# Kernel tuning notes

Measured on AMD Instinct MI355X. Metric: run time of the kernel, lower is better.

Reference implementation:

```python
import jax, jax.numpy as jnp
import numpy as np

D_MODEL = 512
H = 8
D_FF = 2048
EPS = 1e-6
NEG_INF = -1.0e9


def setup_inputs() -> dict:
    key = jax.random.key(0)
    ks = jax.random.split(key, 12)
    B, S, D, F = 8, 2048, D_MODEL, D_FF
    s = 0.02
    inp = {
        "x": jax.random.normal(ks[0], (B, S, D), jnp.float32),
        "src_mask": jnp.ones((B, 1, 1, S), jnp.int32),
        "w_q": jax.random.normal(ks[1], (D, D), jnp.float32) * s,
        "b_q": jnp.zeros((D,), jnp.float32),
        "w_k": jax.random.normal(ks[2], (D, D), jnp.float32) * s,
        "b_k": jnp.zeros((D,), jnp.float32),
        "w_v": jax.random.normal(ks[3], (D, D), jnp.float32) * s,
        "b_v": jnp.zeros((D,), jnp.float32),
        "w_o": jax.random.normal(ks[4], (D, D), jnp.float32) * s,
        "b_o": jnp.zeros((D,), jnp.float32),
        "w_1": jax.random.normal(ks[5], (F, D), jnp.float32) * s,
        "b_1": jnp.zeros((F,), jnp.float32),
        "w_2": jax.random.normal(ks[6], (D, F), jnp.float32) * s,
        "b_2": jnp.zeros((D,), jnp.float32),
    }
    return inp


def _layer_norm(x):
    # Matches torch: (x - mu) / sqrt(std**2 + eps), std is UNBIASED (ddof=1);
    # alpha/bias params exist in the module but are never applied in forward.
    mu = jnp.mean(x, axis=-1, keepdims=True)
    var = jnp.var(x, axis=-1, keepdims=True, ddof=1)
    return (x - mu) / jnp.sqrt(var + EPS)


def _mha(x, src_mask, w_q, b_q, w_k, b_k, w_v, b_v, w_o, b_o):
    B, S, D = x.shape
    d_k = D // H
    q = x @ w_q.T + b_q
    k = x @ w_k.T + b_k
    v = x @ w_v.T + b_v
    # (B, S, H, d_k) -> (B, H, S, d_k)
    q = q.reshape(B, S, H, d_k).transpose(0, 2, 1, 3)
    k = k.reshape(B, S, H, d_k).transpose(0, 2, 1, 3)
    v = v.reshape(B, S, H, d_k).transpose(0, 2, 1, 3)
    scores = jnp.einsum("bhqd,bhkd->bhqk", q, k) / jnp.sqrt(jnp.float32(d_k))
    scores = jnp.where(src_mask == 0, NEG_INF, scores)
    attn = jax.nn.softmax(scores, axis=-1)  # (B, H, S, S) materialized, as in source
    out = jnp.einsum("bhqk,bhkd->bhqd", attn, v)
    out = out.transpose(0, 2, 1, 3).reshape(B, S, D)
    return out @ w_o.T + b_o


def _ffn(x, w_1, b_1, w_2, b_2):
    return jax.nn.relu(x @ w_1.T + b_1) @ w_2.T + b_2


def reference(x, src_mask, w_q, b_q, w_k, b_k, w_v, b_v, w_o, b_o, w_1, b_1, w_2, b_2):
    # dropout prob = 0.0 -> identity (eval-equivalent)
    x1 = x + _mha(_layer_norm(x), src_mask, w_q, b_q, w_k, b_k, w_v, b_v, w_o, b_o)
    return x1 + _ffn(_layer_norm(x1), w_1, b_1, w_2, b_2)
```

## Files before the change

### kernel.cpp

```cpp
#include <hip/hip_runtime.h>
#include <hip/hip_bf16.h>

typedef unsigned short u16;
typedef __bf16 bf16x8 __attribute__((ext_vector_type(8)));
typedef __bf16 bf16x4 __attribute__((ext_vector_type(4)));
typedef unsigned int u32x4 __attribute__((ext_vector_type(4)));
typedef float f32x4 __attribute__((ext_vector_type(4)));

#define SEQ 2048
#define DMODEL 512
#define NHEAD 8
#define DFF 2048
#define NBATCH 8
#define MROWS (NBATCH * SEQ)

#define C1_FOLD 0.18033688f

__device__ __forceinline__ u16 f2b(float f) {
    __hip_bfloat16 h = __float2bfloat16(f);
    u16 u;
    __builtin_memcpy(&u, &h, 2);
    return u;
}

__device__ __forceinline__ unsigned int pack2(float a, float b) {
    float2 f{a, b};
    __hip_bfloat162 h = __float22bfloat162_rn(f);
    unsigned int u;
    __builtin_memcpy(&u, &h, 4);
    return u;
}

__device__ __forceinline__ float ex2(float x) {
#if __has_builtin(__builtin_amdgcn_exp2f)
    return __builtin_amdgcn_exp2f(x);
#else
    return exp2f(x);
#endif
}

__device__ __forceinline__ void gload_lds16(const void* g, void* lds) {
    auto* gp = reinterpret_cast<const __attribute__((address_space(1))) unsigned int*>(
        reinterpret_cast<uintptr_t>(g));
    auto* lp = reinterpret_cast<__attribute__((address_space(3))) unsigned int*>(
        reinterpret_cast<uintptr_t>(lds));
    __builtin_amdgcn_global_load_lds(gp, lp, 16, 0, 0);
}

__global__ __launch_bounds__(256) void cast_weights(
    const float* __restrict__ w0, const float* __restrict__ w1,
    const float* __restrict__ w2, const float* __restrict__ w3,
    const float* __restrict__ w4, const float* __restrict__ w5,
    u16* __restrict__ d0, u16* __restrict__ d1, u16* __restrict__ d2,
    u16* __restrict__ d3, u16* __restrict__ d4, u16* __restrict__ d5) {
    int blk = blockIdx.x;
    const float* s;
    u16* d;
    int base;
    float sc = 1.0f;
    if (blk < 512) {
        int seg = blk >> 7, lb = blk & 127;
        s = seg == 0 ? w0 : seg == 1 ? w1 : seg == 2 ? w2 : w3;
        d = seg == 0 ? d0 : seg == 1 ? d1 : seg == 2 ? d2 : d3;
        base = lb * 2048;
        if (seg == 0) sc = C1_FOLD;
    } else if (blk < 1024) {
        s = w4; d = d4; base = (blk - 512) * 2048;
    } else {
        s = w5; d = d5; base = (blk - 1024) * 2048;
    }
    int i = base + threadIdx.x * 8;
    float4 a = *reinterpret_cast<const float4*>(s + i);
    float4 b = *reinterpret_cast<const float4*>(s + i + 4);
    ushort4 oa, ob;
    oa.x = f2b(a.x * sc); oa.y = f2b(a.y * sc);
    oa.z = f2b(a.z * sc); oa.w = f2b(a.w * sc);
    ob.x = f2b(b.x * sc); ob.y = f2b(b.y * sc);
    ob.z = f2b(b.z * sc); ob.w = f2b(b.w * sc);
    *reinterpret_cast<ushort4*>(d + i) = oa;
    *reinterpret_cast<ushort4*>(d + i + 4) = ob;
}

__global__ __launch_bounds__(256) void concat_bias(const float* __restrict__ bq,
                                                   const float* __restrict__ bk,
                                                   const float* __restrict__ bv,
                                                   float* __restrict__ dst) {
    int i = blockIdx.x * 256 + threadIdx.x;
    float v = i < 512 ? bq[i] * C1_FOLD : (i < 1024 ? bk[i - 512] : bv[i - 1024]);
    dst[i] = v;
}

__global__ __launch_bounds__(256) void ln_rows(const float* __restrict__ x,
                                               u16* __restrict__ out) {
    int row = blockIdx.x * 4 + (threadIdx.x >> 6);
    int l = threadIdx.x & 63;
    const float* xr = x + (size_t)row * DMODEL + l * 8;
    float4 a = *reinterpret_cast<const float4*>(xr);
    float4 b = *reinterpret_cast<const float4*>(xr + 4);
    float s = a.x + a.y + a.z + a.w + b.x + b.y + b.z + b.w;
    float q = a.x * a.x + a.y * a.y + a.z * a.z + a.w * a.w +
              b.x * b.x + b.y * b.y + b.z * b.z + b.w * b.w;
#pragma unroll
    for (int d = 32; d >= 1; d >>= 1) {
        s += __shfl_xor(s, d, 64);
        q += __shfl_xor(q, d, 64);
    }
    float mean = s * (1.f / 512.f);
    float var = (q - 512.f * mean * mean) * (1.f / 511.f);
    float rs = rsqrtf(var + 1e-6f);
    ushort4 o0, o1;
    o0.x = f2b((a.x - mean) * rs); o0.y = f2b((a.y - mean) * rs);
    o0.z = f2b((a.z - mean) * rs); o0.w = f2b((a.w - mean) * rs);
    o1.x = f2b((b.x - mean) * rs); o1.y = f2b((b.y - mean) * rs);
    o1.z = f2b((b.z - mean) * rs); o1.w = f2b((b.w - mean) * rs);
    u16* op = out + (size_t)row * DMODEL + l * 8;
    *reinterpret_cast<ushort4*>(op) = o0;
    *reinterpret_cast<ushort4*>(op + 4) = o1;
}

template <bool RELU, bool RESID, int OUTMODE>
__global__ __launch_bounds__(256, 2) void gemm_nt(
    const u16* __restrict__ A, const u16* __restrict__ W,
    const float* __restrict__ bias, const float* __restrict__ resid,
    void* __restrict__ Cout, void* __restrict__ Cout2, int N, int K) {
    __shared__ u16 Als[2][128 * 64];
    __shared__ u16 Bls[2][128 * 64];
    const int tid = threadIdx.x;
    const int l = tid & 63, w = tid >> 6;
    const int m0 = blockIdx.y * 128;
    const int n0 = blockIdx.x * 128;
    const int wr = (w >> 1) * 64, wc = (w & 1) * 64;
    const int lhi = l >> 4, l15 = l & 15, l7 = l & 7;

    f32x4 acc[4][4] = {};

    const int srow = l >> 3;
    const int scol = ((l & 7) * 8) ^ (srow << 3);

    auto stage = [&](int buf, int kt) {
#pragma unroll
        for (int i = 0; i < 4; ++i) {
            int cc = w * 4 + i;
            int grow = cc * 8 + srow;
            gload_lds16(&A[(size_t)(m0 + grow) * K + kt + scol],
                        &Als[buf][cc * 512]);
            gload_lds16(&W[(size_t)(n0 + grow) * K + kt + scol],
                        &Bls[buf][cc * 512]);
        }
    };

    auto compute = [&](int buf) {
#pragma unroll
        for (int kk = 0; kk < 2; ++kk) {
            const int koff = (kk * 32 + lhi * 8) ^ (l7 << 3);
            bf16x8 af[4], bfr[4];
#pragma unroll
            for (int m = 0; m < 4; ++m)
                af[m] = *reinterpret_cast<const bf16x8*>(
                    &Als[buf][(wr + m * 16 + l15) * 64 + koff]);
#pragma unroll
            for (int n = 0; n < 4; ++n)
                bfr[n] = *reinterpret_cast<const bf16x8*>(
                    &Bls[buf][(wc + n * 16 + l15) * 64 + koff]);
#pragma unroll
            for (int m = 0; m < 4; ++m)
#pragma unroll
                for (int n = 0; n < 4; ++n)
                    acc[m][n] = __builtin_amdgcn_mfma_f32_16x16x32_bf16(
                        af[m], bfr[n], acc[m][n], 0, 0, 0);
        }
    };

    stage(0, 0);
    asm volatile("s_waitcnt vmcnt(0)" ::: "memory");
    __builtin_amdgcn_s_barrier();

    for (int kt = 0; kt < K; kt += 128) {
        if (kt + 64 < K) stage(1, kt + 64);
        __builtin_amdgcn_sched_barrier(0);
        compute(0);
        asm volatile("s_waitcnt vmcnt(0)" ::: "memory");
        __builtin_amdgcn_s_barrier();
        if (kt + 128 < K) stage(0, kt + 128);
        __builtin_amdgcn_sched_barrier(0);
        compute(1);
        asm volatile("s_waitcnt vmcnt(0)" ::: "memory");
        __builtin_amdgcn_s_barrier();
    }

    int colg[4];
    float bv[4];
#pragma unroll
    for (int cn = 0; cn < 4; ++cn) {
        colg[cn] = n0 + wc + cn * 16 + l15;
        bv[cn] = bias[colg[cn]];
    }
#pragma unroll
    for (int am = 0; am < 4; ++am) {
        int rowg = m0 + wr + am * 16 + 4 * lhi;
#pragma unroll
        for (int cn = 0; cn < 4; ++cn) {
            float v[4];
#pragma unroll
            for (int r = 0; r < 4; ++r) {
                float t = acc[am][cn][r] + bv[cn];
                if constexpr (RELU) t = fmaxf(t, 0.f);
                if constexpr (RESID)
                    t += resid[(size_t)(rowg + r) * N + colg[cn]];
                v[r] = t;
            }
            if constexpr (OUTMODE == 0) {
                u16* o = (u16*)Cout;
#pragma unroll
                for (int r = 0; r < 4; ++r)
                    o[(size_t)(rowg + r) * N + colg[cn]] = f2b(v[r]);
            } else if constexpr (OUTMODE == 1) {
                float* o = (float*)Cout;
#pragma unroll
                for (int r = 0; r < 4; ++r)
                    o[(size_t)(rowg + r) * N + colg[cn]] = v[r];
            } else {
                if (n0 < 1024) {
                    u16* o = (u16*)Cout;
#pragma unroll
                    for (int r = 0; r < 4; ++r)
                        o[(size_t)(rowg + r) * 1024 + colg[cn]] = f2b(v[r]);
                } else {
                    u16* o = (u16*)Cout2;
                    int bb = rowg >> 11, sloc = rowg & 2047;
                    int dg = colg[cn] - 1024;
                    ushort4 pk;
                    pk.x = f2b(v[0]); pk.y = f2b(v[1]);
                    pk.z = f2b(v[2]); pk.w = f2b(v[3]);
                    *reinterpret_cast<ushort4*>(
                        &o[(size_t)bb * 1048576 + (size_t)(sloc >> 2) * 2048 +
                           dg * 4]) = pk;
                }
            }
        }
    }
}

__global__ __launch_bounds__(256, 3) void attn_fwd(
    const u16* __restrict__ qk, const u16* __restrict__ v4,
    const int* __restrict__ mask, u16* __restrict__ out) {
    __shared__ u16 Kls[2][64 * 64];
    __shared__ u16 Vls[2][64 * 64];
    const int tid = threadIdx.x;
    const int l = tid & 63, w = tid >> 6;
    const int lhi = l >> 4, l15 = l & 15;
    const int lb = (blockIdx.x & 7) * 128 + (blockIdx.x >> 3);
    const int qt = lb & 15, bh = lb >> 4;
    const int b = bh >> 3, h = bh & 7;
    const int q0 = qt * 128 + w * 32;

    const u16* Qb = qk + (size_t)b * SEQ * 1024 + h * 64;
    const u16* Kb = Qb + 512;
    const u16* Vb4 = v4 + (size_t)b * 1048576 + h * 256;
    const int* Mb = mask + b * SEQ;

    const int srow = l >> 3;
    const int scol = ((l & 7) ^ srow) << 3;

    bf16x8 qf[2][2];
#pragma unroll
    for (int g = 0; g < 2; ++g) {
        size_t qa = (size_t)(q0 + g * 16 + l15) * 1024 + lhi * 8;
        qf[g][0] = *reinterpret_cast<const bf16x8*>(&Qb[qa]);
        qf[g][1] = *reinterpret_cast<const bf16x8*>(&Qb[qa + 32]);
    }

    int allone;
    {
        int acc = 1;
#pragma unroll
        for (int i = 0; i < 8; ++i) {
            int4 mm = *reinterpret_cast<const int4*>(&Mb[l * 32 + i * 4]);
            acc &= mm.x & mm.y & mm.z & mm.w;
        }
        allone = __all(acc == 1);
    }

    float lrun[2] = {0.f, 0.f};
    f32x4 oacc[2][4] = {};

    auto stage = [&](int buf, int kv) {
#pragma unroll
        for (int i = 0; i < 2; ++i) {
            int cc = w * 2 + i;
            int row = cc * 8 + srow;
            gload_lds16(&Kb[(size_t)(kv + row) * 1024 + scol], &Kls[buf][cc * 512]);
            gload_lds16(&Vb4[(size_t)((kv >> 2) + cc * 2 + (l >> 5)) * 2048 +
                             (l & 31) * 8],
                        &Vls[buf][cc * 512]);
        }
    };

    const int sw = (l15 & 7) << 3;

    auto tile = [&](int buf, int kv, bool pf, int pbuf, int pkv) {
        if (pf) stage(pbuf, pkv);
        __builtin_amdgcn_sched_barrier(0);

        f32x4 sc[2][4];
        __builtin_amdgcn_s_setprio(1);
#pragma unroll
        for (int ks = 0; ks < 4; ++ks) {
            int krow = ks * 16 + l15;
            bf16x8 ka0 = *reinterpret_cast<const bf16x8*>(
                &Kls[buf][krow * 64 + ((lhi * 8) ^ sw)]);
            bf16x8 ka1 = *reinterpret_cast<const bf16x8*>(
                &Kls[buf][krow * 64 + ((32 + lhi * 8) ^ sw)]);
#pragma unroll
            for (int g = 0; g < 2; ++g) {
                f32x4 z = {};
                z = __builtin_amdgcn_mfma_f32_16x16x32_bf16(ka0, qf[g][0], z, 0, 0, 0);
                z = __builtin_amdgcn_mfma_f32_16x16x32_bf16(ka1, qf[g][1], z, 0, 0, 0);
                sc[g][ks] = z;
            }
        }
        __builtin_amdgcn_s_setprio(0);

        if (!allone) {
            int4 mm[4];
#pragma unroll
            for (int ks = 0; ks < 4; ++ks)
                mm[ks] = *reinterpret_cast<const int4*>(&Mb[kv + ks * 16 + 4 * lhi]);
#pragma unroll
            for (int ks = 0; ks < 4; ++ks) {
                if (mm[ks].x == 0) { sc[0][ks][0] = -3e38f; sc[1][ks][0] = -3e38f; }
                if (mm[ks].y == 0) { sc[0][ks][1] = -3e38f; sc[1][ks][1] = -3e38f; }
                if (mm[ks].z == 0) { sc[0][ks][2] = -3e38f; sc[1][ks][2] = -3e38f; }
                if (mm[ks].w == 0) { sc[0][ks][3] = -3e38f; sc[1][ks][3] = -3e38f; }
            }
        }

        u32x4 pku[2][2];
#pragma unroll
        for (int g = 0; g < 2; ++g) {
            float ps = 0.f;
#pragma unroll
            for (int ks = 0; ks < 4; ++ks) {
                float p0 = ex2(fminf(sc[g][ks][0], 30.f));
                float p1 = ex2(fminf(sc[g][ks][1], 30.f));
                float p2 = ex2(fminf(sc[g][ks][2], 30.f));
                float p3 = ex2(fminf(sc[g][ks][3], 30.f));
                ps += (p0 + p1) + (p2 + p3);
                pku[g][ks >> 1][(ks & 1) * 2 + 0] = pack2(p0, p1);
                pku[g][ks >> 1][(ks & 1) * 2 + 1] = pack2(p2, p3);
            }
            ps += __shfl_xor(ps, 16, 64);
            ps += __shfl_xor(ps, 32, 64);
            lrun[g] += ps;
        }

        __builtin_amdgcn_s_setprio(1);
#pragma unroll
        for (int kp = 0; kp < 2; ++kp) {
#pragma unroll
            for (int dc = 0; dc < 4; ++dc) {
                int dl4 = (dc * 16 + l15) * 4;
                bf16x4 v0 = *reinterpret_cast<const bf16x4*>(
                    &Vls[buf][(kp * 8 + lhi) * 256 + dl4]);
                bf16x4 v1 = *reinterpret_cast<const bf16x4*>(
                    &Vls[buf][(kp * 8 + 4 + lhi) * 256 + dl4]);
                bf16x8 vb8;
                vb8[0] = v0[0]; vb8[1] = v0[1]; vb8[2] = v0[2]; vb8[3] = v0[3];
                vb8[4] = v1[0]; vb8[5] = v1[1]; vb8[6] = v1[2]; vb8[7] = v1[3];
#pragma unroll
                for (int g = 0; g < 2; ++g)
                    oacc[g][dc] = __builtin_amdgcn_mfma_f32_16x16x32_bf16(
                        __builtin_bit_cast(bf16x8, pku[g][kp]), vb8, oacc[g][dc],
                        0, 0, 0);
            }
        }
        __builtin_amdgcn_s_setprio(0);

        asm volatile("s_waitcnt vmcnt(0)" ::: "memory");
        __builtin_amdgcn_s_barrier();
    };

    stage(0, 0);
    asm volatile("s_waitcnt vmcnt(0)" ::: "memory");
    __builtin_amdgcn_s_barrier();

    for (int tt = 0; tt < 16; ++tt) {
        const int base = tt * 128;
        tile(0, base, true, 1, base + 64);
        tile(1, base + 64, tt < 15, 0, base + 128);
    }

#pragma unroll
    for (int g = 0; g < 2; ++g) {
        float inv = 1.f / lrun[g];
        float invr[4];
#pragma unroll
        for (int r = 0; r < 4; ++r) invr[r] = __shfl(inv, 4 * lhi + r, 16);
#pragma unroll
        for (int r = 0; r < 4; ++r) {
            size_t rowa =
                ((size_t)b * SEQ + q0 + g * 16 + 4 * lhi + r) * DMODEL + h * 64;
#pragma unroll
            for (int dc = 0; dc < 4; ++dc)
                out[rowa + dc * 16 + l15] = f2b(oacc[g][dc][r] * invr[r]);
        }
    }
}

extern "C" void kernel_launch(void* const* d_in, const int* in_sizes, int n_in,
                              void* d_out, int out_size, void* d_ws,
                              size_t ws_size, hipStream_t stream) {
    const float* x = (const float*)d_in[0];
    const int* mask = (const int*)d_in[1];
    const float* w_q = (const float*)d_in[2];
    const float* b_q = (const float*)d_in[3];
    const float* w_k = (const float*)d_in[4];
    const float* b_k = (const float*)d_in[5];
    const float* w_v = (const float*)d_in[6];
    const float* b_v = (const float*)d_in[7];
    const float* w_o = (const float*)d_in[8];
    const float* b_o = (const float*)d_in[9];
    const float* w_1 = (const float*)d_in[10];
    const float* b_1 = (const float*)d_in[11];
    const float* w_2 = (const float*)d_in[12];
    const float* b_2 = (const float*)d_in[13];

    char* ws = (char*)d_ws;
    const size_t MB = 1024ull * 1024ull;
    u16* lnx = (u16*)(ws + 0);
    u16* qkb = (u16*)(ws + 16 * MB);
    u16* v4 = (u16*)(ws + 48 * MB);
    u16* lnx1 = (u16*)(ws + 16 * MB);
    u16* hbuf = (u16*)(ws + 32 * MB);
    u16* wqkv = (u16*)(ws + 96 * MB);
    u16* wob = wqkv + 3 * 262144;
    u16* w1b = wqkv + 4 * 262144;
    u16* w2b = w1b + 1048576;
    float* bqkv = (float*)(w2b + 1048576);
    u16* attn_o = lnx;
    float* x1 = (float*)d_out;

    cast_weights<<<1536, 256, 0, stream>>>(
        w_q, w_k, w_v, w_o, w_1, w_2, wqkv, wqkv + 262144, wqkv + 2 * 262144,
        wob, w1b, w2b);
    concat_bias<<<6, 256, 0, stream>>>(b_q, b_k, b_v, bqkv);
    ln_rows<<<4096, 256, 0, stream>>>(x, lnx);

    dim3 g12(12, 128), g4(4, 128), g16(16, 128);
    gemm_nt<false, false, 3><<<g12, 256, 0, stream>>>(lnx, wqkv, bqkv, nullptr,
                                                      qkb, v4, 1536, 512);
    attn_fwd<<<1024, 256, 0, stream>>>(qkb, v4, mask, attn_o);
    gemm_nt<false, true, 1><<<g4, 256, 0, stream>>>(attn_o, wob, b_o, x, x1,
                                                    nullptr, 512, 512);
    ln_rows<<<4096, 256, 0, stream>>>(x1, lnx1);
    gemm_nt<true, false, 0><<<g16, 256, 0, stream>>>(lnx1, w1b, b_1, nullptr,
                                                     hbuf, nullptr, 2048, 512);
    gemm_nt<false, true, 1><<<g4, 256, 0, stream>>>(hbuf, w2b, b_2, x1,
                                                    (float*)d_out, nullptr,
                                                    512, 2048);
}
```

Measured before the change: 282.5 us.

## Repack V into 8-key groups and compute softmax row sums via MFMA

After: 269.6 us. -4.6%, faster.

```diff
diff --git a/kernel.cpp b/kernel.cpp
--- a/kernel.cpp
+++ b/kernel.cpp
@@ -3,7 +3,6 @@
 
 typedef unsigned short u16;
 typedef __bf16 bf16x8 __attribute__((ext_vector_type(8)));
-typedef __bf16 bf16x4 __attribute__((ext_vector_type(4)));
 typedef unsigned int u32x4 __attribute__((ext_vector_type(4)));
 typedef float f32x4 __attribute__((ext_vector_type(4)));
 
@@ -229,12 +228,13 @@
                     u16* o = (u16*)Cout2;
                     int bb = rowg >> 11, sloc = rowg & 2047;
                     int dg = colg[cn] - 1024;
+                    int kk = sloc >> 5, hb = (sloc >> 4) & 1, ss = (sloc >> 2) & 3;
                     ushort4 pk;
                     pk.x = f2b(v[0]); pk.y = f2b(v[1]);
                     pk.z = f2b(v[2]); pk.w = f2b(v[3]);
                     *reinterpret_cast<ushort4*>(
-                        &o[(size_t)bb * 1048576 + (size_t)(sloc >> 2) * 2048 +
-                           dg * 4]) = pk;
+                        &o[(size_t)(bb * 64 + kk) * 16384 + ss * 4096 + dg * 8 +
+                           hb * 4]) = pk;
                 }
             }
         }
@@ -242,10 +242,10 @@
 }
 
 __global__ __launch_bounds__(256, 3) void attn_fwd(
-    const u16* __restrict__ qk, const u16* __restrict__ v4,
+    const u16* __restrict__ qk, const u16* __restrict__ v8,
     const int* __restrict__ mask, u16* __restrict__ out) {
     __shared__ u16 Kls[2][64 * 64];
-    __shared__ u16 Vls[2][64 * 64];
+    __shared__ u16 Vls[2][8 * 512];
     const int tid = threadIdx.x;
     const int l = tid & 63, w = tid >> 6;
     const int lhi = l >> 4, l15 = l & 15;
@@ -256,7 +256,7 @@
 
     const u16* Qb = qk + (size_t)b * SEQ * 1024 + h * 64;
     const u16* Kb = Qb + 512;
-    const u16* Vb4 = v4 + (size_t)b * 1048576 + h * 256;
+    const u16* Vb8 = v8 + (size_t)b * 1048576 + h * 512;
     const int* Mb = mask + b * SEQ;
 
     const int srow = l >> 3;
@@ -270,6 +270,10 @@
         qf[g][1] = *reinterpret_cast<const bf16x8*>(&Qb[qa + 32]);
     }
 
+    bf16x8 ones8;
+#pragma unroll
+    for (int i = 0; i < 8; ++i) ones8[i] = (__bf16)1.0f;
+
     int allone;
     {
         int acc = 1;
@@ -281,8 +285,8 @@
         allone = __all(acc == 1);
     }
 
-    float lrun[2] = {0.f, 0.f};
     f32x4 oacc[2][4] = {};
+    f32x4 osum[2] = {};
 
     auto stage = [&](int buf, int kv) {
 #pragma unroll
@@ -290,8 +294,8 @@
             int cc = w * 2 + i;
             int row = cc * 8 + srow;
             gload_lds16(&Kb[(size_t)(kv + row) * 1024 + scol], &Kls[buf][cc * 512]);
-            gload_lds16(&Vb4[(size_t)((kv >> 2) + cc * 2 + (l >> 5)) * 2048 +
-                             (l & 31) * 8],
+            gload_lds16(&Vb8[(size_t)((kv >> 5) + (cc >> 2)) * 16384 +
+                             (cc & 3) * 4096 + l * 8],
                         &Vls[buf][cc * 512]);
         }
     };
@@ -338,20 +342,15 @@
         u32x4 pku[2][2];
 #pragma unroll
         for (int g = 0; g < 2; ++g) {
-            float ps = 0.f;
 #pragma unroll
             for (int ks = 0; ks < 4; ++ks) {
                 float p0 = ex2(fminf(sc[g][ks][0], 30.f));
                 float p1 = ex2(fminf(sc[g][ks][1], 30.f));
                 float p2 = ex2(fminf(sc[g][ks][2], 30.f));
                 float p3 = ex2(fminf(sc[g][ks][3], 30.f));
-                ps += (p0 + p1) + (p2 + p3);
                 pku[g][ks >> 1][(ks & 1) * 2 + 0] = pack2(p0, p1);
                 pku[g][ks >> 1][(ks & 1) * 2 + 1] = pack2(p2, p3);
             }
-            ps += __shfl_xor(ps, 16, 64);
-            ps += __shfl_xor(ps, 32, 64);
-            lrun[g] += ps;
         }
 
         __builtin_amdgcn_s_setprio(1);
@@ -359,20 +358,19 @@
         for (int kp = 0; kp < 2; ++kp) {
 #pragma unroll
             for (int dc = 0; dc < 4; ++dc) {
-                int dl4 = (dc * 16 + l15) * 4;
-                bf16x4 v0 = *reinterpret_cast<const bf16x4*>(
-                    &Vls[buf][(kp * 8 + lhi) * 256 + dl4]);
-                bf16x4 v1 = *reinterpret_cast<const bf16x4*>(
-                    &Vls[buf][(kp * 8 + 4 + lhi) * 256 + dl4]);
-                bf16x8 vb8;
-                vb8[0] = v0[0]; vb8[1] = v0[1]; vb8[2] = v0[2]; vb8[3] = v0[3];
-                vb8[4] = v1[0]; vb8[5] = v1[1]; vb8[6] = v1[2]; vb8[7] = v1[3];
+                bf16x8 vb8 = *reinterpret_cast<const bf16x8*>(
+                    &Vls[buf][(kp * 4 + lhi) * 512 + (dc * 16 + l15) * 8]);
 #pragma unroll
                 for (int g = 0; g < 2; ++g)
                     oacc[g][dc] = __builtin_amdgcn_mfma_f32_16x16x32_bf16(
                         __builtin_bit_cast(bf16x8, pku[g][kp]), vb8, oacc[g][dc],
                         0, 0, 0);
             }
+#pragma unroll
+            for (int g = 0; g < 2; ++g)
+                osum[g] = __builtin_amdgcn_mfma_f32_16x16x32_bf16(
+                    __builtin_bit_cast(bf16x8, pku[g][kp]), ones8, osum[g],
+                    0, 0, 0);
         }
         __builtin_amdgcn_s_setprio(0);
 
@@ -392,17 +390,14 @@
 
 #pragma unroll
     for (int g = 0; g < 2; ++g) {
-        float inv = 1.f / lrun[g];
-        float invr[4];
-#pragma unroll
-        for (int r = 0; r < 4; ++r) invr[r] = __shfl(inv, 4 * lhi + r, 16);
 #pragma unroll
         for (int r = 0; r < 4; ++r) {
+            float inv = 1.f / osum[g][r];
             size_t rowa =
                 ((size_t)b * SEQ + q0 + g * 16 + 4 * lhi + r) * DMODEL + h * 64;
 #pragma unroll
             for (int dc = 0; dc < 4; ++dc)
-                out[rowa + dc * 16 + l15] = f2b(oacc[g][dc][r] * invr[r]);
+                out[rowa + dc * 16 + l15] = f2b(oacc[g][dc][r] * inv);
         }
     }
 }
@@ -429,7 +424,7 @@
     const size_t MB = 1024ull * 1024ull;
     u16* lnx = (u16*)(ws + 0);
     u16* qkb = (u16*)(ws + 16 * MB);
-    u16* v4 = (u16*)(ws + 48 * MB);
+    u16* v8 = (u16*)(ws + 48 * MB);
     u16* lnx1 = (u16*)(ws + 16 * MB);
     u16* hbuf = (u16*)(ws + 32 * MB);
     u16* wqkv = (u16*)(ws + 96 * MB);
@@ -448,8 +443,8 @@
 
     dim3 g12(12, 128), g4(4, 128), g16(16, 128);
     gemm_nt<false, false, 3><<<g12, 256, 0, stream>>>(lnx, wqkv, bqkv, nullptr,
-                                                      qkb, v4, 1536, 512);
-    attn_fwd<<<1024, 256, 0, stream>>>(qkb, v4, mask, attn_o);
+                                                      qkb, v8, 1536, 512);
+    attn_fwd<<<1024, 256, 0, stream>>>(qkb, v8, mask, attn_o);
     gemm_nt<false, true, 1><<<g4, 256, 0, stream>>>(attn_o, wob, b_o, x, x1,
                                                     nullptr, 512, 512);
     ln_rows<<<4096, 256, 0, stream>>>(x1, lnx1);
```
